# Optimization experiments

Hardware: AMD Instinct MI355X
Metric: run time of the kernel (lower is better)

The kernel has to match this reference:

```python
import jax, jax.numpy as jnp
import numpy as np

T = 2048        # tokens (single prefill sequence)
H = 4096        # hidden size
NQ = 32         # query heads
NKV = 8         # kv heads
HD = 128        # qk head_dim
VD = 96         # v head_dim (mismatched -> pad/slice path)
WIN = 1024      # sliding window size
E = 8           # routed experts
F = 1408        # moe intermediate
K = 2           # experts per token
EPS = 1e-6
THETA = 1e6


def setup_inputs() -> dict:
    key = jax.random.key(0)
    ks = jax.random.split(key, 10)
    s = 0.02
    return {
        "positions": jnp.arange(T, dtype=jnp.int32),
        "hidden_states": jax.random.normal(ks[0], (T, H), jnp.float32),
        "rms1_w": jnp.ones((H,), jnp.float32),
        "rms2_w": jnp.ones((H,), jnp.float32),
        "wq": jax.random.normal(ks[1], (H, NQ * HD), jnp.float32) * s,
        "wk": jax.random.normal(ks[2], (H, NKV * HD), jnp.float32) * s,
        "wv": jax.random.normal(ks[3], (H, NKV * VD), jnp.float32) * s,
        "wo": jax.random.normal(ks[4], (NQ * VD, H), jnp.float32) * s,
        "sink": jax.random.normal(ks[5], (NQ,), jnp.float32),
        "gate_w": jax.random.normal(ks[6], (H, E), jnp.float32) * s,
        "w_gate": jax.random.normal(ks[7], (E, H, F), jnp.float32) * s,
        "w_up": jax.random.normal(ks[8], (E, H, F), jnp.float32) * s,
        "w_down": jax.random.normal(ks[9], (E, F, H), jnp.float32) * s,
    }


def _rmsnorm(x, w):
    var = jnp.mean(x * x, axis=-1, keepdims=True)
    return x * jax.lax.rsqrt(var + EPS) * w


def _rope(positions, x):
    # neox style, full rotary over HD
    inv_freq = 1.0 / (THETA ** (jnp.arange(0, HD, 2, dtype=jnp.float32) / HD))
    ang = positions.astype(jnp.float32)[:, None] * inv_freq      # [T, HD/2]
    cos = jnp.cos(ang)[:, None, :]                               # [T, 1, HD/2]
    sin = jnp.sin(ang)[:, None, :]
    x1, x2 = x[..., : HD // 2], x[..., HD // 2 :]
    return jnp.concatenate([x1 * cos - x2 * sin, x2 * cos + x1 * sin], axis=-1)


def _forward(positions, hidden_states, rms1_w, rms2_w, wq, wk, wv, wo, sink,
             gate_w, w_gate, w_up, w_down):
    residual = hidden_states
    x = _rmsnorm(hidden_states, rms1_w)

    # ---- attention ----
    q = (x @ wq).reshape(T, NQ, HD)
    k = (x @ wk).reshape(T, NKV, HD)
    v = (x @ wv).reshape(T, NKV, VD)
    q = _rope(positions, q)
    k = _rope(positions, k)
    rep = NQ // NKV
    k = jnp.repeat(k, rep, axis=1)   # [T, NQ, HD]
    v = jnp.repeat(v, rep, axis=1)   # [T, NQ, VD]

    scale = HD ** -0.5
    scores = jnp.einsum('qhd,khd->hqk', q, k) * scale           # [NQ, T, T]
    i = positions[:, None]
    j = positions[None, :]
    mask = (j <= i) & ((i - j) < WIN)                            # causal + sliding window
    scores = jnp.where(mask[None, :, :], scores, jnp.float32(-1e30))
    # attention sink: extra per-head logit contributing only to the denominator
    sink_col = jnp.broadcast_to(sink[:, None, None], (NQ, T, 1))
    logits = jnp.concatenate([scores, sink_col], axis=-1)        # [NQ, T, T+1]
    probs = jax.nn.softmax(logits, axis=-1)[..., :T]
    attn = jnp.einsum('hqk,khv->qhv', probs, v)                  # [T, NQ, VD]
    attn_out = attn.reshape(T, NQ * VD) @ wo                     # [T, H]

    h = residual + attn_out

    # ---- MoE FFN ----
    x2 = _rmsnorm(h, rms2_w)
    router_logits = x2 @ gate_w                                   # [T, E]
    router_probs = jax.nn.softmax(router_logits, axis=-1)
    topk_w, topk_ids = jax.lax.top_k(router_probs, K)             # [T, K]
    topk_w = topk_w / jnp.sum(topk_w, axis=-1, keepdims=True)     # renormalize
    combine = jnp.zeros((T, E), jnp.float32).at[
        jnp.arange(T)[:, None], topk_ids].add(topk_w)             # [T, E]

    h1 = jnp.einsum('td,edf->etf', x2, w_gate)
    h2 = jnp.einsum('td,edf->etf', x2, w_up)
    eo = jnp.einsum('etf,efd->etd', jax.nn.silu(h1) * h2, w_down)  # [E, T, H]
    moe_out = jnp.einsum('etd,te->td', eo, combine)               # [T, H]

    return h + moe_out


def reference(positions, hidden_states, rms1_w, rms2_w, wq, wk, wv, wo, sink,
              gate_w, w_gate, w_up, w_down):
    return _forward(positions, hidden_states, rms1_w, rms2_w, wq, wk, wv, wo,
                    sink, gate_w, w_gate, w_up, w_down)
```

## Files before the change

### kernel.cpp

```cpp
#include <hip/hip_runtime.h>
#include <math.h>

#define T 2048
#define H 4096
#define NQ 32
#define NKV 8
#define HD 128
#define VD 96
#define WIN 1024
#define NE 8
#define FF 1408
#define TOPK 2

typedef __bf16 bf16x8 __attribute__((ext_vector_type(8)));
typedef unsigned short u16x8 __attribute__((ext_vector_type(8)));
typedef float f32x4 __attribute__((ext_vector_type(4)));

__device__ __forceinline__ unsigned short f2bf(float f) {
  union { float f; unsigned u; } v; v.f = f;
  unsigned r = v.u + 0x7fffu + ((v.u >> 16) & 1u);
  return (unsigned short)(r >> 16);
}
__device__ __forceinline__ float bf2f(unsigned short h) {
  union { unsigned u; float f; } v; v.u = ((unsigned)h) << 16;
  return v.f;
}
__device__ __forceinline__ f32x4 mfma16(bf16x8 a, bf16x8 b, f32x4 c) {
  return __builtin_amdgcn_mfma_f32_16x16x32_bf16(a, b, c, 0, 0, 0);
}
__device__ __forceinline__ f32x4 fzero4() { f32x4 z = {0.f, 0.f, 0.f, 0.f}; return z; }

struct Sel3 {
  const float* B[3];
  void* C[3];
  int nbend[3];
  int ldbn[3];
};

template<int SPLIT, int GATHER, int EOFF, int OUTBF, int RES>
__global__ __launch_bounds__(256) void gemm_a16(
    const unsigned short* __restrict__ Ah, const unsigned short* __restrict__ Al,
    int lda, Sel3 sel, long long strideB,
    const float* __restrict__ res,
    const int* __restrict__ row_idx, const int* __restrict__ e_off,
    int M, int K)
{
  __shared__ __align__(16) unsigned short As[SPLIT ? 2 : 1][128][40];
  __shared__ __align__(16) unsigned short Bs[SPLIT ? 2 : 1][128][40];

  int rowbase = 0, Mloc = M;
  if (EOFF) {
    int e = blockIdx.z;
    rowbase = e_off[e];
    Mloc = e_off[e + 1] - rowbase;
  }
  int mtile = blockIdx.y * 128;
  if (mtile >= Mloc) return;

  int nb = blockIdx.x;
  int s = (nb < sel.nbend[0]) ? 0 : ((nb < sel.nbend[1]) ? 1 : 2);
  int nbase = (s == 0) ? 0 : sel.nbend[s - 1];
  int ldb = sel.ldbn[s];
  const float* B = sel.B[s];
  if (EOFF) B += strideB * (long long)blockIdx.z;
  int n0 = (nb - nbase) * 128;

  int tid = threadIdx.x;
  int lane = tid & 63, wave = tid >> 6;
  int g = lane >> 4, cc = lane & 15;
  int wrow = (wave >> 1) * 64, wcol = (wave & 1) * 64;

  f32x4 acc[4][4];
#pragma unroll
  for (int m = 0; m < 4; ++m)
#pragma unroll
    for (int n = 0; n < 4; ++n) acc[m][n] = fzero4();

  const u16x8 z8 = {0, 0, 0, 0, 0, 0, 0, 0};
  int nK = K >> 5;
  for (int kt = 0; kt < nK; ++kt) {
    int k0 = kt << 5;
    __syncthreads();
#pragma unroll
    for (int i = 0; i < 2; ++i) {
      int c = tid + i * 256;
      int row = c >> 2, ks = (c & 3) << 3;
      int grow = mtile + row;
      u16x8 vh = z8, vl = z8;
      if (grow < Mloc) {
        long long ar = rowbase + grow;
        if (GATHER) ar = row_idx[ar];
        vh = *(const u16x8*)(Ah + (size_t)ar * lda + k0 + ks);
        if (SPLIT) vl = *(const u16x8*)(Al + (size_t)ar * lda + k0 + ks);
      }
      *(u16x8*)&As[0][row][ks] = vh;
      if (SPLIT) *(u16x8*)&As[1][row][ks] = vl;
    }
    {
      int nn = (tid & 31) << 2;
      int kb4 = (tid >> 5) << 2;
      const float* bp = B + (size_t)(k0 + kb4) * ldb + n0 + nn;
      float4 r0 = *(const float4*)bp;
      float4 r1 = *(const float4*)(bp + (size_t)ldb);
      float4 r2 = *(const float4*)(bp + 2 * (size_t)ldb);
      float4 r3 = *(const float4*)(bp + 3 * (size_t)ldb);
      ushort4 w;
      w.x = f2bf(r0.x); w.y = f2bf(r1.x); w.z = f2bf(r2.x); w.w = f2bf(r3.x);
      *(ushort4*)&Bs[0][nn + 0][kb4] = w;
      if (SPLIT) {
        ushort4 l; l.x = f2bf(r0.x - bf2f(w.x)); l.y = f2bf(r1.x - bf2f(w.y));
        l.z = f2bf(r2.x - bf2f(w.z)); l.w = f2bf(r3.x - bf2f(w.w));
        *(ushort4*)&Bs[1][nn + 0][kb4] = l;
      }
      w.x = f2bf(r0.y); w.y = f2bf(r1.y); w.z = f2bf(r2.y); w.w = f2bf(r3.y);
      *(ushort4*)&Bs[0][nn + 1][kb4] = w;
      if (SPLIT) {
        ushort4 l; l.x = f2bf(r0.y - bf2f(w.x)); l.y = f2bf(r1.y - bf2f(w.y));
        l.z = f2bf(r2.y - bf2f(w.z)); l.w = f2bf(r3.y - bf2f(w.w));
        *(ushort4*)&Bs[1][nn + 1][kb4] = l;
      }
      w.x = f2bf(r0.z); w.y = f2bf(r1.z); w.z = f2bf(r2.z); w.w = f2bf(r3.z);
      *(ushort4*)&Bs[0][nn + 2][kb4] = w;
      if (SPLIT) {
        ushort4 l; l.x = f2bf(r0.z - bf2f(w.x)); l.y = f2bf(r1.z - bf2f(w.y));
        l.z = f2bf(r2.z - bf2f(w.z)); l.w = f2bf(r3.z - bf2f(w.w));
        *(ushort4*)&Bs[1][nn + 2][kb4] = l;
      }
      w.x = f2bf(r0.w); w.y = f2bf(r1.w); w.z = f2bf(r2.w); w.w = f2bf(r3.w);
      *(ushort4*)&Bs[0][nn + 3][kb4] = w;
      if (SPLIT) {
        ushort4 l; l.x = f2bf(r0.w - bf2f(w.x)); l.y = f2bf(r1.w - bf2f(w.y));
        l.z = f2bf(r2.w - bf2f(w.z)); l.w = f2bf(r3.w - bf2f(w.w));
        *(ushort4*)&Bs[1][nn + 3][kb4] = l;
      }
    }
    __syncthreads();
    bf16x8 avh[4], bvh[4], avl[4], bvl[4];
#pragma unroll
    for (int m = 0; m < 4; ++m) {
      avh[m] = *(const bf16x8*)&As[0][wrow + m * 16 + cc][g * 8];
      if (SPLIT) avl[m] = *(const bf16x8*)&As[1][wrow + m * 16 + cc][g * 8];
    }
#pragma unroll
    for (int n = 0; n < 4; ++n) {
      bvh[n] = *(const bf16x8*)&Bs[0][wcol + n * 16 + cc][g * 8];
      if (SPLIT) bvl[n] = *(const bf16x8*)&Bs[1][wcol + n * 16 + cc][g * 8];
    }
#pragma unroll
    for (int m = 0; m < 4; ++m)
#pragma unroll
      for (int n = 0; n < 4; ++n) {
        acc[m][n] = mfma16(avh[m], bvh[n], acc[m][n]);
        if (SPLIT) {
          acc[m][n] = mfma16(avh[m], bvl[n], acc[m][n]);
          acc[m][n] = mfma16(avl[m], bvh[n], acc[m][n]);
        }
      }
  }

  int ldc = ldb;
#pragma unroll
  for (int m = 0; m < 4; ++m) {
    int rl = wrow + m * 16 + g * 4;
#pragma unroll
    for (int n = 0; n < 4; ++n) {
      int col = n0 + wcol + n * 16 + cc;
#pragma unroll
      for (int r = 0; r < 4; ++r) {
        int grow = mtile + rl + r;
        if (grow < Mloc) {
          size_t off = (size_t)(rowbase + grow) * ldc + col;
          float vv = acc[m][n][r];
          if (OUTBF) {
            ((unsigned short*)sel.C[s])[off] = f2bf(vv);
          } else {
            if (RES) vv += res[off];
            ((float*)sel.C[s])[off] = vv;
          }
        }
      }
    }
  }
}

__global__ __launch_bounds__(256) void rmsnorm_hl_kernel(const float* __restrict__ in,
    const float* __restrict__ w, unsigned short* __restrict__ oh,
    unsigned short* __restrict__ ol)
{
  int t = blockIdx.x;
  int tid = threadIdx.x;
  const float4* rp = (const float4*)(in + (size_t)t * H);
  const float4* wp = (const float4*)w;
  float4 vv[4];
  float ss = 0.f;
#pragma unroll
  for (int i = 0; i < 4; ++i) {
    vv[i] = rp[tid + i * 256];
    ss += vv[i].x * vv[i].x + vv[i].y * vv[i].y + vv[i].z * vv[i].z + vv[i].w * vv[i].w;
  }
#pragma unroll
  for (int off = 32; off > 0; off >>= 1) ss += __shfl_xor(ss, off);
  __shared__ float red[4];
  if ((tid & 63) == 0) red[tid >> 6] = ss;
  __syncthreads();
  float tot = red[0] + red[1] + red[2] + red[3];
  float rs = rsqrtf(tot * (1.f / H) + 1e-6f);
#pragma unroll
  for (int i = 0; i < 4; ++i) {
    float4 x = vv[i];
    float4 ww = wp[tid + i * 256];
    float y0 = x.x * rs * ww.x, y1 = x.y * rs * ww.y;
    float y2 = x.z * rs * ww.z, y3 = x.w * rs * ww.w;
    ushort4 hh, ll;
    hh.x = f2bf(y0); hh.y = f2bf(y1); hh.z = f2bf(y2); hh.w = f2bf(y3);
    ll.x = f2bf(y0 - bf2f(hh.x)); ll.y = f2bf(y1 - bf2f(hh.y));
    ll.z = f2bf(y2 - bf2f(hh.z)); ll.w = f2bf(y3 - bf2f(hh.w));
    *(ushort4*)&oh[(size_t)t * H + (tid + i * 256) * 4] = hh;
    *(ushort4*)&ol[(size_t)t * H + (tid + i * 256) * 4] = ll;
  }
}

__global__ __launch_bounds__(256) void rmsnorm_fh_kernel(const float* __restrict__ in,
    const float* __restrict__ w, float* __restrict__ of,
    unsigned short* __restrict__ oh)
{
  int t = blockIdx.x;
  int tid = threadIdx.x;
  const float4* rp = (const float4*)(in + (size_t)t * H);
  const float4* wp = (const float4*)w;
  float4 vv[4];
  float ss = 0.f;
#pragma unroll
  for (int i = 0; i < 4; ++i) {
    vv[i] = rp[tid + i * 256];
    ss += vv[i].x * vv[i].x + vv[i].y * vv[i].y + vv[i].z * vv[i].z + vv[i].w * vv[i].w;
  }
#pragma unroll
  for (int off = 32; off > 0; off >>= 1) ss += __shfl_xor(ss, off);
  __shared__ float red[4];
  if ((tid & 63) == 0) red[tid >> 6] = ss;
  __syncthreads();
  float tot = red[0] + red[1] + red[2] + red[3];
  float rs = rsqrtf(tot * (1.f / H) + 1e-6f);
#pragma unroll
  for (int i = 0; i < 4; ++i) {
    float4 x = vv[i];
    float4 ww = wp[tid + i * 256];
    float4 o;
    o.x = x.x * rs * ww.x; o.y = x.y * rs * ww.y;
    o.z = x.z * rs * ww.z; o.w = x.w * rs * ww.w;
    *(float4*)&of[(size_t)t * H + (tid + i * 256) * 4] = o;
    ushort4 hh;
    hh.x = f2bf(o.x); hh.y = f2bf(o.y); hh.z = f2bf(o.z); hh.w = f2bf(o.w);
    *(ushort4*)&oh[(size_t)t * H + (tid + i * 256) * 4] = hh;
  }
}

__global__ __launch_bounds__(256) void rope_pack_kernel(const int* __restrict__ pos,
    const float* __restrict__ qf, const float* __restrict__ kf, const float* __restrict__ vf,
    unsigned short* __restrict__ qh, unsigned short* __restrict__ ql,
    unsigned short* __restrict__ kh, unsigned short* __restrict__ kl,
    unsigned short* __restrict__ vh, unsigned short* __restrict__ vl)
{
  int t = blockIdx.x;
  float p = (float)pos[t];
  int tid = threadIdx.x;
  for (int idx = tid; idx < (NQ + NKV) * 64; idx += 256) {
    const float* src; unsigned short *dh, *dl; size_t base; int d;
    if (idx < NQ * 64) {
      int hh = idx >> 6; d = idx & 63;
      base = (size_t)t * (NQ * HD) + hh * HD;
      src = qf; dh = qh; dl = ql;
    } else {
      int j = idx - NQ * 64;
      int hh = j >> 6; d = j & 63;
      base = (size_t)t * (NKV * HD) + hh * HD;
      src = kf; dh = kh; dl = kl;
    }
    float inv = exp2f(-19.931568569324174f * (float)(2 * d) * (1.0f / 128.0f));
    float ang = p * inv;
    float sn = sinf(ang), cs = cosf(ang);
    float x1 = src[base + d], x2 = src[base + d + 64];
    float o1 = x1 * cs - x2 * sn;
    float o2 = x2 * cs + x1 * sn;
    unsigned short h1 = f2bf(o1), h2 = f2bf(o2);
    dh[base + d] = h1; dl[base + d] = f2bf(o1 - bf2f(h1));
    dh[base + d + 64] = h2; dl[base + d + 64] = f2bf(o2 - bf2f(h2));
  }
  for (int idx = tid; idx < NKV * VD; idx += 256) {
    size_t o = (size_t)t * (NKV * VD) + idx;
    float v = vf[o];
    unsigned short hh = f2bf(v);
    vh[o] = hh; vl[o] = f2bf(v - bf2f(hh));
  }
}

__global__ __launch_bounds__(256) void attn_kernel(
    const unsigned short* __restrict__ qh, const unsigned short* __restrict__ ql,
    const unsigned short* __restrict__ kh, const unsigned short* __restrict__ kl,
    const unsigned short* __restrict__ vhp, const unsigned short* __restrict__ vlp,
    const float* __restrict__ sink, const int* __restrict__ pos,
    unsigned short* __restrict__ aoh, unsigned short* __restrict__ aol)
{
  __shared__ __align__(16) unsigned short Qs[2][64][136];
  __shared__ __align__(16) unsigned short Ks[2][32][136];
  __shared__ __align__(16) unsigned short Vt[2][96][40];
  __shared__ __align__(16) unsigned short Ps[2][4][16][40];
  __shared__ int posq[64];
  __shared__ int posk[32];

  const float SCALE = 0.08838834764831843f;
  int qs = blockIdx.x * 64;
  int head = blockIdx.y;
  int kvh = head >> 2;
  int tid = threadIdx.x;
  int lane = tid & 63, wave = tid >> 6;
  int g = lane >> 4, cc = lane & 15;
  int wq0 = wave * 16;

#pragma unroll
  for (int i = 0; i < 4; ++i) {
    int c = tid + i * 256;
    int row = c >> 4, ks = (c & 15) << 3;
    size_t gofs = (size_t)(qs + row) * (NQ * HD) + head * HD + ks;
    *(u16x8*)&Qs[0][row][ks] = *(const u16x8*)(qh + gofs);
    *(u16x8*)&Qs[1][row][ks] = *(const u16x8*)(ql + gofs);
  }
  if (tid < 64) posq[tid] = pos[qs + tid];

  float m_r[4], l_r[4];
  f32x4 acc_o[6];
#pragma unroll
  for (int r = 0; r < 4; ++r) { m_r[r] = -__builtin_huge_valf(); l_r[r] = 0.f; }
#pragma unroll
  for (int n = 0; n < 6; ++n) acc_o[n] = fzero4();

  int kstart = qs - (WIN - 1);
  if (kstart < 0) kstart = 0;
  kstart &= ~31;
  int kend = qs + 63;

  for (int k0 = kstart; k0 <= kend; k0 += 32) {
    __syncthreads();
#pragma unroll
    for (int i = 0; i < 2; ++i) {
      int c = tid + i * 256;
      int row = c >> 4, ks = (c & 15) << 3;
      size_t gofs = (size_t)(k0 + row) * (NKV * HD) + kvh * HD + ks;
      *(u16x8*)&Ks[0][row][ks] = *(const u16x8*)(kh + gofs);
      *(u16x8*)&Ks[1][row][ks] = *(const u16x8*)(kl + gofs);
    }
#pragma unroll
    for (int i = 0; i < 3; ++i) {
      int qd = tid + i * 256;
      int key = qd / 24, vq = qd % 24;
      size_t gofs = (size_t)(k0 + key) * (NKV * VD) + kvh * VD + vq * 4;
      ushort4 a = *(const ushort4*)(vhp + gofs);
      ushort4 b = *(const ushort4*)(vlp + gofs);
      Vt[0][vq * 4 + 0][key] = a.x; Vt[0][vq * 4 + 1][key] = a.y;
      Vt[0][vq * 4 + 2][key] = a.z; Vt[0][vq * 4 + 3][key] = a.w;
      Vt[1][vq * 4 + 0][key] = b.x; Vt[1][vq * 4 + 1][key] = b.y;
      Vt[1][vq * 4 + 2][key] = b.z; Vt[1][vq * 4 + 3][key] = b.w;
    }
    if (tid < 32) posk[tid] = pos[k0 + tid];
    __syncthreads();

    bf16x8 aqh[4], aql[4];
#pragma unroll
    for (int kk = 0; kk < 4; ++kk) {
      aqh[kk] = *(const bf16x8*)&Qs[0][wq0 + cc][kk * 32 + g * 8];
      aql[kk] = *(const bf16x8*)&Qs[1][wq0 + cc][kk * 32 + g * 8];
    }
    f32x4 sacc[2];
    sacc[0] = fzero4(); sacc[1] = fzero4();
#pragma unroll
    for (int kb = 0; kb < 2; ++kb)
#pragma unroll
      for (int kk = 0; kk < 4; ++kk) {
        bf16x8 bh = *(const bf16x8*)&Ks[0][kb * 16 + cc][kk * 32 + g * 8];
        bf16x8 bl = *(const bf16x8*)&Ks[1][kb * 16 + cc][kk * 32 + g * 8];
        sacc[kb] = mfma16(aqh[kk], bh, sacc[kb]);
        sacc[kb] = mfma16(aqh[kk], bl, sacc[kb]);
        sacc[kb] = mfma16(aql[kk], bh, sacc[kb]);
      }

    int j0 = posk[cc], j1 = posk[16 + cc];
#pragma unroll
    for (int r = 0; r < 4; ++r) {
      int irow = posq[wq0 + g * 4 + r];
      float s0 = sacc[0][r] * SCALE;
      float s1 = sacc[1][r] * SCALE;
      bool ok0 = (j0 <= irow) && (irow - j0 < WIN);
      bool ok1 = (j1 <= irow) && (irow - j1 < WIN);
      if (!ok0) s0 = -1e30f;
      if (!ok1) s1 = -1e30f;
      float rm = fmaxf(s0, s1);
#pragma unroll
      for (int off = 1; off < 16; off <<= 1) rm = fmaxf(rm, __shfl_xor(rm, off));
      float mn = fmaxf(m_r[r], rm);
      float p0 = ok0 ? __expf(s0 - mn) : 0.f;
      float p1 = ok1 ? __expf(s1 - mn) : 0.f;
      float rs = p0 + p1;
#pragma unroll
      for (int off = 1; off < 16; off <<= 1) rs += __shfl_xor(rs, off);
      float alpha = __expf(m_r[r] - mn);
      l_r[r] = l_r[r] * alpha + rs;
      m_r[r] = mn;
#pragma unroll
      for (int n = 0; n < 6; ++n) acc_o[n][r] *= alpha;
      unsigned short p0h = f2bf(p0), p1h = f2bf(p1);
      Ps[0][wave][g * 4 + r][cc] = p0h;
      Ps[1][wave][g * 4 + r][cc] = f2bf(p0 - bf2f(p0h));
      Ps[0][wave][g * 4 + r][16 + cc] = p1h;
      Ps[1][wave][g * 4 + r][16 + cc] = f2bf(p1 - bf2f(p1h));
    }
    bf16x8 pah = *(const bf16x8*)&Ps[0][wave][cc][g * 8];
    bf16x8 pal = *(const bf16x8*)&Ps[1][wave][cc][g * 8];
#pragma unroll
    for (int n = 0; n < 6; ++n) {
      bf16x8 bh = *(const bf16x8*)&Vt[0][n * 16 + cc][g * 8];
      bf16x8 bl = *(const bf16x8*)&Vt[1][n * 16 + cc][g * 8];
      acc_o[n] = mfma16(pah, bh, acc_o[n]);
      acc_o[n] = mfma16(pah, bl, acc_o[n]);
      acc_o[n] = mfma16(pal, bh, acc_o[n]);
    }
  }

  float snk = sink[head];
#pragma unroll
  for (int r = 0; r < 4; ++r) {
    float m2 = fmaxf(m_r[r], snk);
    float alpha = __expf(m_r[r] - m2);
    float denom = l_r[r] * alpha + __expf(snk - m2);
    float inv = 1.f / denom;
    int row = qs + wq0 + g * 4 + r;
#pragma unroll
    for (int n = 0; n < 6; ++n) {
      float val = acc_o[n][r] * alpha * inv;
      size_t off = (size_t)row * (NQ * VD) + head * VD + n * 16 + cc;
      unsigned short hh = f2bf(val);
      aoh[off] = hh;
      aol[off] = f2bf(val - bf2f(hh));
    }
  }
}

__global__ __launch_bounds__(64) void router_kernel(const float* __restrict__ x2,
    const float* __restrict__ gw, float* __restrict__ topkw, int* __restrict__ topkid)
{
  int t = blockIdx.x;
  int lane = threadIdx.x;
  float acc[NE];
#pragma unroll
  for (int e = 0; e < NE; ++e) acc[e] = 0.f;
  for (int hh = lane; hh < H; hh += 64) {
    float xv = x2[(size_t)t * H + hh];
    const float* g = gw + (size_t)hh * NE;
#pragma unroll
    for (int e = 0; e < NE; ++e) acc[e] = fmaf(xv, g[e], acc[e]);
  }
#pragma unroll
  for (int e = 0; e < NE; ++e)
#pragma unroll
    for (int off = 32; off > 0; off >>= 1) acc[e] += __shfl_xor(acc[e], off);
  if (lane == 0) {
    int b1 = 0; float v1 = acc[0];
#pragma unroll
    for (int e = 1; e < NE; ++e) { if (acc[e] > v1) { v1 = acc[e]; b1 = e; } }
    int b2 = -1; float v2 = -3.4e38f;
#pragma unroll
    for (int e = 0; e < NE; ++e) { if (e != b1 && acc[e] > v2) { v2 = acc[e]; b2 = e; } }
    float e2 = __expf(v2 - v1);
    float s = 1.f + e2;
    topkw[t * 2] = 1.f / s;
    topkw[t * 2 + 1] = e2 / s;
    topkid[t * 2] = b1;
    topkid[t * 2 + 1] = b2;
  }
}

__global__ __launch_bounds__(256) void route_build_kernel(
    const int* __restrict__ topkid, int* __restrict__ idssort,
    int* __restrict__ prow, int* __restrict__ eoffs)
{
  __shared__ int cnt[NE];
  __shared__ int off[NE + 1];
  __shared__ int cur[NE];
  int tid = threadIdx.x;
  if (tid < NE) cnt[tid] = 0;
  __syncthreads();
  for (int p = tid; p < T * TOPK; p += 256) atomicAdd(&cnt[topkid[p]], 1);
  __syncthreads();
  if (tid == 0) {
    off[0] = 0;
    for (int e = 0; e < NE; ++e) off[e + 1] = off[e] + cnt[e];
  }
  __syncthreads();
  if (tid < NE) cur[tid] = off[tid];
  __syncthreads();
  for (int p = tid; p < T * TOPK; p += 256) {
    int e = topkid[p];
    int ppos = atomicAdd(&cur[e], 1);
    idssort[ppos] = p >> 1;
    prow[p] = ppos;
  }
  if (tid <= NE) eoffs[tid] = off[tid];
}

__global__ __launch_bounds__(256) void silu_mul_kernel(
    const unsigned short* __restrict__ h1b, const unsigned short* __restrict__ h2b,
    unsigned short* __restrict__ oh, int n8)
{
  int i = blockIdx.x * 256 + threadIdx.x;
  if (i < n8) {
    ushort4 a0 = ((const ushort4*)h1b)[i * 2], a1 = ((const ushort4*)h1b)[i * 2 + 1];
    ushort4 b0 = ((const ushort4*)h2b)[i * 2], b1 = ((const ushort4*)h2b)[i * 2 + 1];
    ushort4 o0, o1;
    float x, y, r;
    x = bf2f(a0.x); y = bf2f(b0.x); r = x / (1.f + __expf(-x)) * y; o0.x = f2bf(r);
    x = bf2f(a0.y); y = bf2f(b0.y); r = x / (1.f + __expf(-x)) * y; o0.y = f2bf(r);
    x = bf2f(a0.z); y = bf2f(b0.z); r = x / (1.f + __expf(-x)) * y; o0.z = f2bf(r);
    x = bf2f(a0.w); y = bf2f(b0.w); r = x / (1.f + __expf(-x)) * y; o0.w = f2bf(r);
    x = bf2f(a1.x); y = bf2f(b1.x); r = x / (1.f + __expf(-x)) * y; o1.x = f2bf(r);
    x = bf2f(a1.y); y = bf2f(b1.y); r = x / (1.f + __expf(-x)) * y; o1.y = f2bf(r);
    x = bf2f(a1.z); y = bf2f(b1.z); r = x / (1.f + __expf(-x)) * y; o1.z = f2bf(r);
    x = bf2f(a1.w); y = bf2f(b1.w); r = x / (1.f + __expf(-x)) * y; o1.w = f2bf(r);
    ((ushort4*)oh)[i * 2] = o0;
    ((ushort4*)oh)[i * 2 + 1] = o1;
  }
}

__global__ __launch_bounds__(256) void combine_kernel(const float* __restrict__ h,
    const float* __restrict__ eo, const float* __restrict__ topkw,
    const int* __restrict__ prow, float* __restrict__ out)
{
  int t = blockIdx.x, tid = threadIdx.x;
  float w0 = topkw[t * 2], w1 = topkw[t * 2 + 1];
  const float4* e0 = (const float4*)(eo + (size_t)prow[t * 2] * H);
  const float4* e1 = (const float4*)(eo + (size_t)prow[t * 2 + 1] * H);
  const float4* hp = (const float4*)(h + (size_t)t * H);
  float4* op = (float4*)(out + (size_t)t * H);
#pragma unroll
  for (int i = 0; i < 4; ++i) {
    int idx = tid + i * 256;
    float4 a = hp[idx], b = e0[idx], c = e1[idx];
    float4 o;
    o.x = a.x + w0 * b.x + w1 * c.x;
    o.y = a.y + w0 * b.y + w1 * c.y;
    o.z = a.z + w0 * b.z + w1 * c.z;
    o.w = a.w + w0 * b.w + w1 * c.w;
    op[idx] = o;
  }
}

extern "C" void kernel_launch(void* const* d_in, const int* in_sizes, int n_in,
                              void* d_out, int out_size, void* d_ws, size_t ws_size,
                              hipStream_t stream) {
  const int*   pos   = (const int*)d_in[0];
  const float* hid   = (const float*)d_in[1];
  const float* rms1w = (const float*)d_in[2];
  const float* rms2w = (const float*)d_in[3];
  const float* wq    = (const float*)d_in[4];
  const float* wk    = (const float*)d_in[5];
  const float* wv    = (const float*)d_in[6];
  const float* wo    = (const float*)d_in[7];
  const float* sink  = (const float*)d_in[8];
  const float* gw    = (const float*)d_in[9];
  const float* wgate = (const float*)d_in[10];
  const float* wup   = (const float*)d_in[11];
  const float* wdown = (const float*)d_in[12];
  float* out = (float*)d_out;

  char* ws = (char*)d_ws;
  const size_t MB = 1048576ull;
  unsigned short* x1h = (unsigned short*)(ws + 0 * MB);
  unsigned short* x1l = (unsigned short*)(ws + 16 * MB);
  float* qf  = (float*)(ws + 32 * MB);
  float* kbf = (float*)(ws + 64 * MB);
  float* vbf = (float*)(ws + 72 * MB);
  unsigned short* qh = (unsigned short*)(ws + 0 * MB);
  unsigned short* ql = (unsigned short*)(ws + 16 * MB);
  unsigned short* kh = (unsigned short*)(ws + 80 * MB);
  unsigned short* kl = (unsigned short*)(ws + 84 * MB);
  unsigned short* vh = (unsigned short*)(ws + 88 * MB);
  unsigned short* vl = (unsigned short*)(ws + 91 * MB);
  unsigned short* aoh = (unsigned short*)(ws + 94 * MB);
  unsigned short* aol = (unsigned short*)(ws + 106 * MB);
  float* h   = (float*)(ws + 118 * MB);
  float* x2  = (float*)(ws + 32 * MB);
  unsigned short* x2h = (unsigned short*)(ws + 64 * MB);
  unsigned short* h1b = (unsigned short*)(ws + 150 * MB);
  unsigned short* h2b = (unsigned short*)(ws + 162 * MB);
  unsigned short* h1h = (unsigned short*)(ws + 80 * MB);
  float* eo  = (float*)(ws + 0 * MB);
  char* sm = ws + 174 * MB;
  float* topkw  = (float*)(sm);
  int*  topkid  = (int*)(sm + 16384);
  int*  prow    = (int*)(sm + 32768);
  int*  idssort = (int*)(sm + 49152);
  int*  eoffs   = (int*)(sm + 65536);

  rmsnorm_hl_kernel<<<T, 256, 0, stream>>>(hid, rms1w, x1h, x1l);

  {
    Sel3 sel;
    sel.B[0] = wq;  sel.B[1] = wk;  sel.B[2] = wv;
    sel.C[0] = qf;  sel.C[1] = kbf; sel.C[2] = vbf;
    sel.nbend[0] = 32; sel.nbend[1] = 40; sel.nbend[2] = 46;
    sel.ldbn[0] = NQ * HD; sel.ldbn[1] = NKV * HD; sel.ldbn[2] = NKV * VD;
    gemm_a16<1, 0, 0, 0, 0><<<dim3(46, 16, 1), 256, 0, stream>>>(
        x1h, x1l, H, sel, 0, nullptr, nullptr, nullptr, T, H);
  }

  rope_pack_kernel<<<T, 256, 0, stream>>>(pos, qf, kbf, vbf, qh, ql, kh, kl, vh, vl);

  attn_kernel<<<dim3(T / 64, NQ, 1), 256, 0, stream>>>(qh, ql, kh, kl, vh, vl,
      sink, pos, aoh, aol);

  {
    Sel3 sel;
    sel.B[0] = wo; sel.B[1] = wo; sel.B[2] = wo;
    sel.C[0] = h;  sel.C[1] = h;  sel.C[2] = h;
    sel.nbend[0] = 32; sel.nbend[1] = 32; sel.nbend[2] = 32;
    sel.ldbn[0] = H; sel.ldbn[1] = H; sel.ldbn[2] = H;
    gemm_a16<1, 0, 0, 0, 1><<<dim3(32, 16, 1), 256, 0, stream>>>(
        aoh, aol, NQ * VD, sel, 0, hid, nullptr, nullptr, T, NQ * VD);
  }

  rmsnorm_fh_kernel<<<T, 256, 0, stream>>>(h, rms2w, x2, x2h);

  router_kernel<<<T, 64, 0, stream>>>(x2, gw, topkw, topkid);
  route_build_kernel<<<1, 256, 0, stream>>>(topkid, idssort, prow, eoffs);

  {
    Sel3 sel;
    sel.B[0] = wgate; sel.B[1] = wup; sel.B[2] = wup;
    sel.C[0] = h1b;   sel.C[1] = h2b; sel.C[2] = h2b;
    sel.nbend[0] = 11; sel.nbend[1] = 22; sel.nbend[2] = 22;
    sel.ldbn[0] = FF; sel.ldbn[1] = FF; sel.ldbn[2] = FF;
    gemm_a16<0, 1, 1, 1, 0><<<dim3(22, 32, 8), 256, 0, stream>>>(
        x2h, nullptr, H, sel, (long long)H * FF, nullptr, idssort, eoffs, 0, H);
  }
  silu_mul_kernel<<<(T * TOPK * FF / 8 + 255) / 256, 256, 0, stream>>>(
      h1b, h2b, h1h, T * TOPK * FF / 8);
  {
    Sel3 sel;
    sel.B[0] = wdown; sel.B[1] = wdown; sel.B[2] = wdown;
    sel.C[0] = eo;    sel.C[1] = eo;   sel.C[2] = eo;
    sel.nbend[0] = 32; sel.nbend[1] = 32; sel.nbend[2] = 32;
    sel.ldbn[0] = H; sel.ldbn[1] = H; sel.ldbn[2] = H;
    gemm_a16<0, 0, 1, 0, 0><<<dim3(32, 32, 8), 256, 0, stream>>>(
        h1h, nullptr, FF, sel, (long long)FF * H, nullptr, nullptr, eoffs, 0, FF);
  }

  combine_kernel<<<T, 256, 0, stream>>>(h, eo, topkw, prow, out);
}
```

Before: 1.638 ms.

## Pre-transpose weights to bf16 and stream GEMM tiles via direct global-to-LDS loads

Adds a transpose-and-convert pass that writes every weight matrix as bf16 (with hi/lo splits where needed) in K-contiguous layout, so the GEMMs no longer convert fp32 B tiles per block. The GEMM now fills LDS with global_load_lds 16-byte copies for both operands, using an unpadded layout. QKV and gate/up outputs become single fused buffers, and rope and silu read them directly. The cost is extra weight conversion traffic on every call, plus possible LDS bank conflicts from dropping the padding.

After: 1.523 ms. 1.08x faster.

```diff
diff --git a/kernel.cpp b/kernel.cpp
--- a/kernel.cpp
+++ b/kernel.cpp
@@ -15,6 +15,7 @@
 typedef __bf16 bf16x8 __attribute__((ext_vector_type(8)));
 typedef unsigned short u16x8 __attribute__((ext_vector_type(8)));
 typedef float f32x4 __attribute__((ext_vector_type(4)));
+typedef unsigned short ushort_t;
 
 __device__ __forceinline__ unsigned short f2bf(float f) {
   union { float f; unsigned u; } v; v.f = f;
@@ -30,121 +31,141 @@
 }
 __device__ __forceinline__ f32x4 fzero4() { f32x4 z = {0.f, 0.f, 0.f, 0.f}; return z; }
 
-struct Sel3 {
-  const float* B[3];
-  void* C[3];
-  int nbend[3];
-  int ldbn[3];
-};
+__device__ __forceinline__ void gl16(const void* g, void* l) {
+  __builtin_amdgcn_global_load_lds(
+      (const __attribute__((address_space(1))) void*)g,
+      (__attribute__((address_space(3))) void*)l, 16, 0, 0);
+}
+
+template<int SPLITOUT>
+__global__ __launch_bounds__(256) void tconv_kernel(
+    const float* __restrict__ src, int ldsrc,
+    ushort_t* __restrict__ dh, ushort_t* __restrict__ dl,
+    int lddst, int dro, long long sE, long long dE)
+{
+  __shared__ float tile[64][65];
+  int e = blockIdx.z;
+  src += sE * (long long)e;
+  dh += dE * (long long)e;
+  if (SPLITOUT) dl += dE * (long long)e;
+  int c0 = blockIdx.x * 64;
+  int r0 = blockIdx.y * 64;
+  int tid = threadIdx.x;
+#pragma unroll
+  for (int i = 0; i < 4; ++i) {
+    int idx = tid + i * 256;
+    int r = idx >> 4, c4 = (idx & 15) << 2;
+    float4 v = *(const float4*)&src[(size_t)(r0 + r) * ldsrc + c0 + c4];
+    tile[r][c4 + 0] = v.x; tile[r][c4 + 1] = v.y;
+    tile[r][c4 + 2] = v.z; tile[r][c4 + 3] = v.w;
+  }
+  __syncthreads();
+#pragma unroll
+  for (int i = 0; i < 2; ++i) {
+    int idx = tid + i * 256;
+    int c = idx >> 3, r8 = (idx & 7) << 3;
+    u16x8 hv, lv;
+#pragma unroll
+    for (int j = 0; j < 8; ++j) {
+      float f = tile[r8 + j][c];
+      unsigned short hh = f2bf(f);
+      hv[j] = hh;
+      if (SPLITOUT) lv[j] = f2bf(f - bf2f(hh));
+    }
+    size_t o = (size_t)(dro + c0 + c) * lddst + r0 + r8;
+    *(u16x8*)&dh[o] = hv;
+    if (SPLITOUT) *(u16x8*)&dl[o] = lv;
+  }
+}
 
 template<int SPLIT, int GATHER, int EOFF, int OUTBF, int RES>
-__global__ __launch_bounds__(256) void gemm_a16(
-    const unsigned short* __restrict__ Ah, const unsigned short* __restrict__ Al,
-    int lda, Sel3 sel, long long strideB,
+__global__ __launch_bounds__(256) void gemm_bt(
+    const ushort_t* __restrict__ Ah, const ushort_t* __restrict__ Al, int lda,
+    const ushort_t* __restrict__ Bh, const ushort_t* __restrict__ Bl,
+    long long strideBe,
+    void* __restrict__ Cp, int ldc,
     const float* __restrict__ res,
     const int* __restrict__ row_idx, const int* __restrict__ e_off,
     int M, int K)
 {
-  __shared__ __align__(16) unsigned short As[SPLIT ? 2 : 1][128][40];
-  __shared__ __align__(16) unsigned short Bs[SPLIT ? 2 : 1][128][40];
+  __shared__ __align__(16) ushort_t As[(SPLIT ? 2 : 1) * 4096];
+  __shared__ __align__(16) ushort_t Bs[(SPLIT ? 2 : 1) * 4096];
 
   int rowbase = 0, Mloc = M;
   if (EOFF) {
     int e = blockIdx.z;
     rowbase = e_off[e];
     Mloc = e_off[e + 1] - rowbase;
+    Bh += strideBe * (long long)e;
+    if (SPLIT) Bl += strideBe * (long long)e;
   }
   int mtile = blockIdx.y * 128;
   if (mtile >= Mloc) return;
-
-  int nb = blockIdx.x;
-  int s = (nb < sel.nbend[0]) ? 0 : ((nb < sel.nbend[1]) ? 1 : 2);
-  int nbase = (s == 0) ? 0 : sel.nbend[s - 1];
-  int ldb = sel.ldbn[s];
-  const float* B = sel.B[s];
-  if (EOFF) B += strideB * (long long)blockIdx.z;
-  int n0 = (nb - nbase) * 128;
+  int n0 = blockIdx.x * 128;
 
   int tid = threadIdx.x;
   int lane = tid & 63, wave = tid >> 6;
   int g = lane >> 4, cc = lane & 15;
   int wrow = (wave >> 1) * 64, wcol = (wave & 1) * 64;
 
+  int ks = (tid & 3) << 3;
+  const ushort_t *aph0, *aph1, *apl0 = nullptr, *apl1 = nullptr;
+  {
+    int r0 = (tid >> 2), r1 = (tid >> 2) + 64;
+    long long ar0, ar1;
+    if (EOFF || GATHER) {
+      int g0 = mtile + r0; if (g0 >= Mloc) g0 = 0;
+      int g1 = mtile + r1; if (g1 >= Mloc) g1 = 0;
+      if (GATHER) { ar0 = row_idx[rowbase + g0]; ar1 = row_idx[rowbase + g1]; }
+      else { ar0 = rowbase + g0; ar1 = rowbase + g1; }
+    } else {
+      ar0 = mtile + r0; ar1 = mtile + r1;
+    }
+    aph0 = Ah + ar0 * lda + ks;
+    aph1 = Ah + ar1 * lda + ks;
+    if (SPLIT) { apl0 = Al + ar0 * lda + ks; apl1 = Al + ar1 * lda + ks; }
+  }
+  const ushort_t* bph0 = Bh + (size_t)(n0 + (tid >> 2)) * K + ks;
+  const ushort_t* bph1 = Bh + (size_t)(n0 + (tid >> 2) + 64) * K + ks;
+  const ushort_t* bpl0 = SPLIT ? Bl + (size_t)(n0 + (tid >> 2)) * K + ks : nullptr;
+  const ushort_t* bpl1 = SPLIT ? Bl + (size_t)(n0 + (tid >> 2) + 64) * K + ks : nullptr;
+  ushort_t* la0 = As + tid * 8;
+  ushort_t* la1 = As + (tid + 256) * 8;
+  ushort_t* lb0 = Bs + tid * 8;
+  ushort_t* lb1 = Bs + (tid + 256) * 8;
+
   f32x4 acc[4][4];
 #pragma unroll
   for (int m = 0; m < 4; ++m)
 #pragma unroll
     for (int n = 0; n < 4; ++n) acc[m][n] = fzero4();
 
-  const u16x8 z8 = {0, 0, 0, 0, 0, 0, 0, 0};
   int nK = K >> 5;
   for (int kt = 0; kt < nK; ++kt) {
     int k0 = kt << 5;
-    __syncthreads();
-#pragma unroll
-    for (int i = 0; i < 2; ++i) {
-      int c = tid + i * 256;
-      int row = c >> 2, ks = (c & 3) << 3;
-      int grow = mtile + row;
-      u16x8 vh = z8, vl = z8;
-      if (grow < Mloc) {
-        long long ar = rowbase + grow;
-        if (GATHER) ar = row_idx[ar];
-        vh = *(const u16x8*)(Ah + (size_t)ar * lda + k0 + ks);
-        if (SPLIT) vl = *(const u16x8*)(Al + (size_t)ar * lda + k0 + ks);
-      }
-      *(u16x8*)&As[0][row][ks] = vh;
-      if (SPLIT) *(u16x8*)&As[1][row][ks] = vl;
-    }
-    {
-      int nn = (tid & 31) << 2;
-      int kb4 = (tid >> 5) << 2;
-      const float* bp = B + (size_t)(k0 + kb4) * ldb + n0 + nn;
-      float4 r0 = *(const float4*)bp;
-      float4 r1 = *(const float4*)(bp + (size_t)ldb);
-      float4 r2 = *(const float4*)(bp + 2 * (size_t)ldb);
-      float4 r3 = *(const float4*)(bp + 3 * (size_t)ldb);
-      ushort4 w;
-      w.x = f2bf(r0.x); w.y = f2bf(r1.x); w.z = f2bf(r2.x); w.w = f2bf(r3.x);
-      *(ushort4*)&Bs[0][nn + 0][kb4] = w;
-      if (SPLIT) {
-        ushort4 l; l.x = f2bf(r0.x - bf2f(w.x)); l.y = f2bf(r1.x - bf2f(w.y));
-        l.z = f2bf(r2.x - bf2f(w.z)); l.w = f2bf(r3.x - bf2f(w.w));
-        *(ushort4*)&Bs[1][nn + 0][kb4] = l;
-      }
-      w.x = f2bf(r0.y); w.y = f2bf(r1.y); w.z = f2bf(r2.y); w.w = f2bf(r3.y);
-      *(ushort4*)&Bs[0][nn + 1][kb4] = w;
-      if (SPLIT) {
-        ushort4 l; l.x = f2bf(r0.y - bf2f(w.x)); l.y = f2bf(r1.y - bf2f(w.y));
-        l.z = f2bf(r2.y - bf2f(w.z)); l.w = f2bf(r3.y - bf2f(w.w));
-        *(ushort4*)&Bs[1][nn + 1][kb4] = l;
-      }
-      w.x = f2bf(r0.z); w.y = f2bf(r1.z); w.z = f2bf(r2.z); w.w = f2bf(r3.z);
-      *(ushort4*)&Bs[0][nn + 2][kb4] = w;
-      if (SPLIT) {
-        ushort4 l; l.x = f2bf(r0.z - bf2f(w.x)); l.y = f2bf(r1.z - bf2f(w.y));
-        l.z = f2bf(r2.z - bf2f(w.z)); l.w = f2bf(r3.z - bf2f(w.w));
-        *(ushort4*)&Bs[1][nn + 2][kb4] = l;
-      }
-      w.x = f2bf(r0.w); w.y = f2bf(r1.w); w.z = f2bf(r2.w); w.w = f2bf(r3.w);
-      *(ushort4*)&Bs[0][nn + 3][kb4] = w;
-      if (SPLIT) {
-        ushort4 l; l.x = f2bf(r0.w - bf2f(w.x)); l.y = f2bf(r1.w - bf2f(w.y));
-        l.z = f2bf(r2.w - bf2f(w.z)); l.w = f2bf(r3.w - bf2f(w.w));
-        *(ushort4*)&Bs[1][nn + 3][kb4] = l;
-      }
+    gl16(aph0 + k0, la0);
+    gl16(aph1 + k0, la1);
+    gl16(bph0 + k0, lb0);
+    gl16(bph1 + k0, lb1);
+    if (SPLIT) {
+      gl16(apl0 + k0, la0 + 4096);
+      gl16(apl1 + k0, la1 + 4096);
+      gl16(bpl0 + k0, lb0 + 4096);
+      gl16(bpl1 + k0, lb1 + 4096);
     }
     __syncthreads();
     bf16x8 avh[4], bvh[4], avl[4], bvl[4];
 #pragma unroll
     for (int m = 0; m < 4; ++m) {
-      avh[m] = *(const bf16x8*)&As[0][wrow + m * 16 + cc][g * 8];
-      if (SPLIT) avl[m] = *(const bf16x8*)&As[1][wrow + m * 16 + cc][g * 8];
+      int row = wrow + m * 16 + cc;
+      avh[m] = *(const bf16x8*)&As[row * 32 + g * 8];
+      if (SPLIT) avl[m] = *(const bf16x8*)&As[4096 + row * 32 + g * 8];
     }
 #pragma unroll
     for (int n = 0; n < 4; ++n) {
-      bvh[n] = *(const bf16x8*)&Bs[0][wcol + n * 16 + cc][g * 8];
-      if (SPLIT) bvl[n] = *(const bf16x8*)&Bs[1][wcol + n * 16 + cc][g * 8];
+      int row = wcol + n * 16 + cc;
+      bvh[n] = *(const bf16x8*)&Bs[row * 32 + g * 8];
+      if (SPLIT) bvl[n] = *(const bf16x8*)&Bs[4096 + row * 32 + g * 8];
     }
 #pragma unroll
     for (int m = 0; m < 4; ++m)
@@ -156,9 +177,9 @@
           acc[m][n] = mfma16(avl[m], bvh[n], acc[m][n]);
         }
       }
-  }
-
-  int ldc = ldb;
+    __syncthreads();
+  }
+
 #pragma unroll
   for (int m = 0; m < 4; ++m) {
     int rl = wrow + m * 16 + g * 4;
@@ -172,10 +193,10 @@
           size_t off = (size_t)(rowbase + grow) * ldc + col;
           float vv = acc[m][n][r];
           if (OUTBF) {
-            ((unsigned short*)sel.C[s])[off] = f2bf(vv);
+            ((ushort_t*)Cp)[off] = f2bf(vv);
           } else {
             if (RES) vv += res[off];
-            ((float*)sel.C[s])[off] = vv;
+            ((float*)Cp)[off] = vv;
           }
         }
       }
@@ -184,8 +205,7 @@
 }
 
 __global__ __launch_bounds__(256) void rmsnorm_hl_kernel(const float* __restrict__ in,
-    const float* __restrict__ w, unsigned short* __restrict__ oh,
-    unsigned short* __restrict__ ol)
+    const float* __restrict__ w, ushort_t* __restrict__ oh, ushort_t* __restrict__ ol)
 {
   int t = blockIdx.x;
   int tid = threadIdx.x;
@@ -221,8 +241,7 @@
 }
 
 __global__ __launch_bounds__(256) void rmsnorm_fh_kernel(const float* __restrict__ in,
-    const float* __restrict__ w, float* __restrict__ of,
-    unsigned short* __restrict__ oh)
+    const float* __restrict__ w, float* __restrict__ of, ushort_t* __restrict__ oh)
 {
   int t = blockIdx.x;
   int tid = threadIdx.x;
@@ -257,55 +276,58 @@
 }
 
 __global__ __launch_bounds__(256) void rope_pack_kernel(const int* __restrict__ pos,
-    const float* __restrict__ qf, const float* __restrict__ kf, const float* __restrict__ vf,
-    unsigned short* __restrict__ qh, unsigned short* __restrict__ ql,
-    unsigned short* __restrict__ kh, unsigned short* __restrict__ kl,
-    unsigned short* __restrict__ vh, unsigned short* __restrict__ vl)
+    const float* __restrict__ qkv,
+    ushort_t* __restrict__ qh, ushort_t* __restrict__ ql,
+    ushort_t* __restrict__ kh, ushort_t* __restrict__ kl,
+    ushort_t* __restrict__ vh, ushort_t* __restrict__ vl)
 {
   int t = blockIdx.x;
   float p = (float)pos[t];
   int tid = threadIdx.x;
+  const float* row = qkv + (size_t)t * 5888;
   for (int idx = tid; idx < (NQ + NKV) * 64; idx += 256) {
-    const float* src; unsigned short *dh, *dl; size_t base; int d;
+    int col; ushort_t *dh, *dl; size_t dbase; int d;
     if (idx < NQ * 64) {
       int hh = idx >> 6; d = idx & 63;
-      base = (size_t)t * (NQ * HD) + hh * HD;
-      src = qf; dh = qh; dl = ql;
+      col = hh * HD + d;
+      dbase = (size_t)t * (NQ * HD) + hh * HD;
+      dh = qh; dl = ql;
     } else {
       int j = idx - NQ * 64;
       int hh = j >> 6; d = j & 63;
-      base = (size_t)t * (NKV * HD) + hh * HD;
-      src = kf; dh = kh; dl = kl;
+      col = 4096 + hh * HD + d;
+      dbase = (size_t)t * (NKV * HD) + hh * HD;
+      dh = kh; dl = kl;
     }
     float inv = exp2f(-19.931568569324174f * (float)(2 * d) * (1.0f / 128.0f));
     float ang = p * inv;
     float sn = sinf(ang), cs = cosf(ang);
-    float x1 = src[base + d], x2 = src[base + d + 64];
+    float x1 = row[col], x2 = row[col + 64];
     float o1 = x1 * cs - x2 * sn;
     float o2 = x2 * cs + x1 * sn;
     unsigned short h1 = f2bf(o1), h2 = f2bf(o2);
-    dh[base + d] = h1; dl[base + d] = f2bf(o1 - bf2f(h1));
-    dh[base + d + 64] = h2; dl[base + d + 64] = f2bf(o2 - bf2f(h2));
+    dh[dbase + d] = h1; dl[dbase + d] = f2bf(o1 - bf2f(h1));
+    dh[dbase + d + 64] = h2; dl[dbase + d + 64] = f2bf(o2 - bf2f(h2));
   }
   for (int idx = tid; idx < NKV * VD; idx += 256) {
+    float v = row[5120 + idx];
     size_t o = (size_t)t * (NKV * VD) + idx;
-    float v = vf[o];
     unsigned short hh = f2bf(v);
     vh[o] = hh; vl[o] = f2bf(v - bf2f(hh));
   }
 }
 
 __global__ __launch_bounds__(256) void attn_kernel(
-    const unsigned short* __restrict__ qh, const unsigned short* __restrict__ ql,
-    const unsigned short* __restrict__ kh, const unsigned short* __restrict__ kl,
-    const unsigned short* __restrict__ vhp, const unsigned short* __restrict__ vlp,
+    const ushort_t* __restrict__ qh, const ushort_t* __restrict__ ql,
+    const ushort_t* __restrict__ kh, const ushort_t* __restrict__ kl,
+    const ushort_t* __restrict__ vhp, const ushort_t* __restrict__ vlp,
     const float* __restrict__ sink, const int* __restrict__ pos,
-    unsigned short* __restrict__ aoh, unsigned short* __restrict__ aol)
-{
-  __shared__ __align__(16) unsigned short Qs[2][64][136];
-  __shared__ __align__(16) unsigned short Ks[2][32][136];
-  __shared__ __align__(16) unsigned short Vt[2][96][40];
-  __shared__ __align__(16) unsigned short Ps[2][4][16][40];
+    ushort_t* __restrict__ aoh, ushort_t* __restrict__ aol)
+{
+  __shared__ __align__(16) ushort_t Qs[2][64][136];
+  __shared__ __align__(16) ushort_t Ks[2][32][136];
+  __shared__ __align__(16) ushort_t Vt[2][96][40];
+  __shared__ __align__(16) ushort_t Ps[2][4][16][40];
   __shared__ int posq[64];
   __shared__ int posk[32];
 
@@ -508,26 +530,21 @@
 }
 
 __global__ __launch_bounds__(256) void silu_mul_kernel(
-    const unsigned short* __restrict__ h1b, const unsigned short* __restrict__ h2b,
-    unsigned short* __restrict__ oh, int n8)
-{
-  int i = blockIdx.x * 256 + threadIdx.x;
-  if (i < n8) {
-    ushort4 a0 = ((const ushort4*)h1b)[i * 2], a1 = ((const ushort4*)h1b)[i * 2 + 1];
-    ushort4 b0 = ((const ushort4*)h2b)[i * 2], b1 = ((const ushort4*)h2b)[i * 2 + 1];
-    ushort4 o0, o1;
-    float x, y, r;
-    x = bf2f(a0.x); y = bf2f(b0.x); r = x / (1.f + __expf(-x)) * y; o0.x = f2bf(r);
-    x = bf2f(a0.y); y = bf2f(b0.y); r = x / (1.f + __expf(-x)) * y; o0.y = f2bf(r);
-    x = bf2f(a0.z); y = bf2f(b0.z); r = x / (1.f + __expf(-x)) * y; o0.z = f2bf(r);
-    x = bf2f(a0.w); y = bf2f(b0.w); r = x / (1.f + __expf(-x)) * y; o0.w = f2bf(r);
-    x = bf2f(a1.x); y = bf2f(b1.x); r = x / (1.f + __expf(-x)) * y; o1.x = f2bf(r);
-    x = bf2f(a1.y); y = bf2f(b1.y); r = x / (1.f + __expf(-x)) * y; o1.y = f2bf(r);
-    x = bf2f(a1.z); y = bf2f(b1.z); r = x / (1.f + __expf(-x)) * y; o1.z = f2bf(r);
-    x = bf2f(a1.w); y = bf2f(b1.w); r = x / (1.f + __expf(-x)) * y; o1.w = f2bf(r);
-    ((ushort4*)oh)[i * 2] = o0;
-    ((ushort4*)oh)[i * 2 + 1] = o1;
-  }
+    const ushort_t* __restrict__ h12, ushort_t* __restrict__ oh)
+{
+  int id = blockIdx.x * 256 + threadIdx.x;
+  int r = id / 176;
+  int c8 = (id % 176) * 8;
+  u16x8 a = *(const u16x8*)&h12[(size_t)r * 2816 + c8];
+  u16x8 b = *(const u16x8*)&h12[(size_t)r * 2816 + 1408 + c8];
+  u16x8 o;
+#pragma unroll
+  for (int j = 0; j < 8; ++j) {
+    float x = bf2f(a[j]), y = bf2f(b[j]);
+    float rr = x / (1.f + __expf(-x)) * y;
+    o[j] = f2bf(rr);
+  }
+  *(u16x8*)&oh[(size_t)r * 1408 + c8] = o;
 }
 
 __global__ __launch_bounds__(256) void combine_kernel(const float* __restrict__ h,
@@ -571,87 +588,75 @@
   const float* wdown = (const float*)d_in[12];
   float* out = (float*)d_out;
 
+  const size_t MB = 1048576ull;
+  if (ws_size < 462ull * MB) return;
+
   char* ws = (char*)d_ws;
-  const size_t MB = 1048576ull;
-  unsigned short* x1h = (unsigned short*)(ws + 0 * MB);
-  unsigned short* x1l = (unsigned short*)(ws + 16 * MB);
-  float* qf  = (float*)(ws + 32 * MB);
-  float* kbf = (float*)(ws + 64 * MB);
-  float* vbf = (float*)(ws + 72 * MB);
-  unsigned short* qh = (unsigned short*)(ws + 0 * MB);
-  unsigned short* ql = (unsigned short*)(ws + 16 * MB);
-  unsigned short* kh = (unsigned short*)(ws + 80 * MB);
-  unsigned short* kl = (unsigned short*)(ws + 84 * MB);
-  unsigned short* vh = (unsigned short*)(ws + 88 * MB);
-  unsigned short* vl = (unsigned short*)(ws + 91 * MB);
-  unsigned short* aoh = (unsigned short*)(ws + 94 * MB);
-  unsigned short* aol = (unsigned short*)(ws + 106 * MB);
-  float* h   = (float*)(ws + 118 * MB);
-  float* x2  = (float*)(ws + 32 * MB);
-  unsigned short* x2h = (unsigned short*)(ws + 64 * MB);
-  unsigned short* h1b = (unsigned short*)(ws + 150 * MB);
-  unsigned short* h2b = (unsigned short*)(ws + 162 * MB);
-  unsigned short* h1h = (unsigned short*)(ws + 80 * MB);
-  float* eo  = (float*)(ws + 0 * MB);
-  char* sm = ws + 174 * MB;
+  ushort_t* wqkvT_h = (ushort_t*)(ws + 0 * MB);
+  ushort_t* wqkvT_l = (ushort_t*)(ws + 47 * MB);
+  ushort_t* woT_h   = (ushort_t*)(ws + 94 * MB);
+  ushort_t* woT_l   = (ushort_t*)(ws + 118 * MB);
+  ushort_t* wgupT   = (ushort_t*)(ws + 0 * MB);
+  ushort_t* wdownT  = (ushort_t*)(ws + 176 * MB);
+  char* A0 = ws + 264 * MB;
+  ushort_t* x1h = (ushort_t*)(A0 + 0 * MB);
+  ushort_t* x1l = (ushort_t*)(A0 + 16 * MB);
+  ushort_t* kh  = (ushort_t*)(A0 + 32 * MB);
+  ushort_t* kl  = (ushort_t*)(A0 + 36 * MB);
+  ushort_t* vh  = (ushort_t*)(A0 + 40 * MB);
+  ushort_t* vl  = (ushort_t*)(A0 + 43 * MB);
+  ushort_t* aoh = (ushort_t*)(A0 + 46 * MB);
+  ushort_t* aol = (ushort_t*)(A0 + 58 * MB);
+  ushort_t* qh  = (ushort_t*)(A0 + 0 * MB);
+  ushort_t* ql  = (ushort_t*)(A0 + 16 * MB);
+  float* eo   = (float*)(A0 + 0 * MB);
+  float* qkvf = (float*)(A0 + 70 * MB);
+  ushort_t* h12b = (ushort_t*)(A0 + 70 * MB);
+  ushort_t* h1h  = (ushort_t*)(A0 + 93 * MB);
+  float* h   = (float*)(A0 + 116 * MB);
+  float* x2  = (float*)(A0 + 148 * MB);
+  ushort_t* x2h = (ushort_t*)(A0 + 180 * MB);
+  char* sm = A0 + 196 * MB;
   float* topkw  = (float*)(sm);
   int*  topkid  = (int*)(sm + 16384);
   int*  prow    = (int*)(sm + 32768);
   int*  idssort = (int*)(sm + 49152);
   int*  eoffs   = (int*)(sm + 65536);
 
+  tconv_kernel<1><<<dim3(64, 64, 1), 256, 0, stream>>>(wq, 4096, wqkvT_h, wqkvT_l, 4096, 0, 0, 0);
+  tconv_kernel<1><<<dim3(16, 64, 1), 256, 0, stream>>>(wk, 1024, wqkvT_h, wqkvT_l, 4096, 4096, 0, 0);
+  tconv_kernel<1><<<dim3(12, 64, 1), 256, 0, stream>>>(wv, 768, wqkvT_h, wqkvT_l, 4096, 5120, 0, 0);
+  tconv_kernel<1><<<dim3(64, 48, 1), 256, 0, stream>>>(wo, 4096, woT_h, woT_l, 3072, 0, 0, 0);
+  tconv_kernel<0><<<dim3(64, 22, 8), 256, 0, stream>>>(wdown, 4096, wdownT, nullptr, 1408, 0,
+      1408LL * 4096, 4096LL * 1408);
+
   rmsnorm_hl_kernel<<<T, 256, 0, stream>>>(hid, rms1w, x1h, x1l);
 
-  {
-    Sel3 sel;
-    sel.B[0] = wq;  sel.B[1] = wk;  sel.B[2] = wv;
-    sel.C[0] = qf;  sel.C[1] = kbf; sel.C[2] = vbf;
-    sel.nbend[0] = 32; sel.nbend[1] = 40; sel.nbend[2] = 46;
-    sel.ldbn[0] = NQ * HD; sel.ldbn[1] = NKV * HD; sel.ldbn[2] = NKV * VD;
-    gemm_a16<1, 0, 0, 0, 0><<<dim3(46, 16, 1), 256, 0, stream>>>(
-        x1h, x1l, H, sel, 0, nullptr, nullptr, nullptr, T, H);
-  }
-
-  rope_pack_kernel<<<T, 256, 0, stream>>>(pos, qf, kbf, vbf, qh, ql, kh, kl, vh, vl);
+  gemm_bt<1, 0, 0, 0, 0><<<dim3(46, 16, 1), 256, 0, stream>>>(
+      x1h, x1l, H, wqkvT_h, wqkvT_l, 0, qkvf, 5888, nullptr, nullptr, nullptr, T, H);
+
+  rope_pack_kernel<<<T, 256, 0, stream>>>(pos, qkvf, qh, ql, kh, kl, vh, vl);
 
   attn_kernel<<<dim3(T / 64, NQ, 1), 256, 0, stream>>>(qh, ql, kh, kl, vh, vl,
       sink, pos, aoh, aol);
 
-  {
-    Sel3 sel;
-    sel.B[0] = wo; sel.B[1] = wo; sel.B[2] = wo;
-    sel.C[0] = h;  sel.C[1] = h;  sel.C[2] = h;
-    sel.nbend[0] = 32; sel.nbend[1] = 32; sel.nbend[2] = 32;
-    sel.ldbn[0] = H; sel.ldbn[1] = H; sel.ldbn[2] = H;
-    gemm_a16<1, 0, 0, 0, 1><<<dim3(32, 16, 1), 256, 0, stream>>>(
-        aoh, aol, NQ * VD, sel, 0, hid, nullptr, nullptr, T, NQ * VD);
-  }
+  gemm_bt<1, 0, 0, 0, 1><<<dim3(32, 16, 1), 256, 0, stream>>>(
+      aoh, aol, NQ * VD, woT_h, woT_l, 0, h, H, hid, nullptr, nullptr, T, NQ * VD);
 
   rmsnorm_fh_kernel<<<T, 256, 0, stream>>>(h, rms2w, x2, x2h);
 
   router_kernel<<<T, 64, 0, stream>>>(x2, gw, topkw, topkid);
   route_build_kernel<<<1, 256, 0, stream>>>(topkid, idssort, prow, eoffs);
 
-  {
-    Sel3 sel;
-    sel.B[0] = wgate; sel.B[1] = wup; sel.B[2] = wup;
-    sel.C[0] = h1b;   sel.C[1] = h2b; sel.C[2] = h2b;
-    sel.nbend[0] = 11; sel.nbend[1] = 22; sel.nbend[2] = 22;
-    sel.ldbn[0] = FF; sel.ldbn[1] = FF; sel.ldbn[2] = FF;
-    gemm_a16<0, 1, 1, 1, 0><<<dim3(22, 32, 8), 256, 0, stream>>>(
-        x2h, nullptr, H, sel, (long long)H * FF, nullptr, idssort, eoffs, 0, H);
-  }
-  silu_mul_kernel<<<(T * TOPK * FF / 8 + 255) / 256, 256, 0, stream>>>(
-      h1b, h2b, h1h, T * TOPK * FF / 8);
-  {
-    Sel3 sel;
-    sel.B[0] = wdown; sel.B[1] = wdown; sel.B[2] = wdown;
-    sel.C[0] = eo;    sel.C[1] = eo;   sel.C[2] = eo;
-    sel.nbend[0] = 32; sel.nbend[1] = 32; sel.nbend[2] = 32;
-    sel.ldbn[0] = H; sel.ldbn[1] = H; sel.ldbn[2] = H;
-    gemm_a16<0, 0, 1, 0, 0><<<dim3(32, 32, 8), 256, 0, stream>>>(
-        h1h, nullptr, FF, sel, (long long)FF * H, nullptr, nullptr, eoffs, 0, FF);
-  }
+  tconv_kernel<0><<<dim3(22, 64, 8), 256, 0, stream>>>(wgate, 1408, wgupT, nullptr, 4096, 0,
+      4096LL * 1408, 2816LL * 4096);
+  tconv_kernel<0><<<dim3(22, 64, 8), 256, 0, stream>>>(wup, 1408, wgupT, nullptr, 4096, 1408,
+      4096LL * 1408, 2816LL * 4096);
+  gemm_bt<0, 1, 1, 1, 0><<<dim3(22, 32, 8), 256, 0, stream>>>(
+      x2h, nullptr, H, wgupT, nullptr, 2816LL * 4096, h12b, 2816, nullptr, idssort, eoffs, 0, H);
+  silu_mul_kernel<<<2816, 256, 0, stream>>>(h12b, h1h);
+  gemm_bt<0, 0, 1, 0, 0><<<dim3(32, 32, 8), 256, 0, stream>>>(
+      h1h, nullptr, FF, wdownT, nullptr, 4096LL * 1408, eo, H, nullptr, nullptr, eoffs, 0, FF);
 
   combine_kernel<<<T, 256, 0, stream>>>(h, eo, topkw, prow, out);
 }
```
